# Kernel optimization log

Measured on AMD Instinct MI355X. Metric: run time of the kernel, lower is better.

The kernel has to match this reference:

```python
import jax, jax.numpy as jnp
import numpy as np

B, S, D, H, L = 32, 2048, 256, 256, 2  # batch, seq_len, input_size, hidden_size, num_layers


def setup_inputs() -> dict:
    key = jax.random.key(0)
    ks = jax.random.split(key, 11)
    s = 0.05
    return {
        "x": jax.random.normal(ks[0], (B, S, D), jnp.float32),
        "enc_h": jax.random.normal(ks[1], (B, 2 * H), jnp.float32),
        "enc_c": jax.random.normal(ks[2], (B, 2 * H), jnp.float32),
        # stacked per-layer LSTMCell params, PyTorch gate order (i, f, g, o)
        "Wih_f": jax.random.normal(ks[3], (L, 4 * H, D), jnp.float32) * s,
        "Whh_f": jax.random.normal(ks[4], (L, 4 * H, H), jnp.float32) * s,
        "bih_f": jax.random.normal(ks[5], (L, 4 * H), jnp.float32) * s,
        "bhh_f": jax.random.normal(ks[6], (L, 4 * H), jnp.float32) * s,
        "Wih_b": jax.random.normal(ks[7], (L, 4 * H, D), jnp.float32) * s,
        "Whh_b": jax.random.normal(ks[8], (L, 4 * H, H), jnp.float32) * s,
        "bih_b": jax.random.normal(ks[9], (L, 4 * H), jnp.float32) * s,
        "bhh_b": jax.random.normal(ks[10], (L, 4 * H), jnp.float32) * s,
    }


def _lstm_cell(x, h, c, Wih, Whh, b):
    gates = x @ Wih.T + h @ Whh.T + b  # [B, 4H]
    i, f, g, o = jnp.split(gates, 4, axis=-1)
    c_new = jax.nn.sigmoid(f) * c + jax.nn.sigmoid(i) * jnp.tanh(g)
    h_new = jax.nn.sigmoid(o) * jnp.tanh(c_new)
    return h_new, c_new


def reference(x, enc_h, enc_c, Wih_f, Whh_f, bih_f, bhh_f, Wih_b, Whh_b, bih_b, bhh_b):
    h = enc_h.shape[1] // 2
    nl = Wih_f.shape[0]
    # initial states: same encoder slice replicated to every layer
    hf0 = jnp.broadcast_to(enc_h[:, :h], (nl, enc_h.shape[0], h))
    hb0 = jnp.broadcast_to(enc_h[:, h:], (nl, enc_h.shape[0], h))
    cf0 = jnp.broadcast_to(enc_c[:, :h], (nl, enc_c.shape[0], h))
    cb0 = jnp.broadcast_to(enc_c[:, h:], (nl, enc_c.shape[0], h))

    def step(carry, x_t):
        hf, cf, hb, cb = carry  # each [L, B, H]
        inp_f = x_t
        inp_b = x_t[:, ::-1]  # source flips the FEATURE axis of the timestep
        hfs, cfs, hbs, cbs = [], [], [], []
        for j in range(nl):
            h_f, c_f = _lstm_cell(inp_f, hf[j], cf[j], Wih_f[j], Whh_f[j], bih_f[j] + bhh_f[j])
            h_b, c_b = _lstm_cell(inp_b, hb[j], cb[j], Wih_b[j], Whh_b[j], bih_b[j] + bhh_b[j])
            inp_f, inp_b = h_f, h_b
            hfs.append(h_f); cfs.append(c_f); hbs.append(h_b); cbs.append(c_b)
        new_carry = (jnp.stack(hfs), jnp.stack(cfs), jnp.stack(hbs), jnp.stack(cbs))
        return new_carry, jnp.concatenate([hfs[-1], hbs[-1]], axis=1)  # [B, 2H]

    carry0 = (hf0, cf0, hb0, cb0)
    xs = jnp.swapaxes(x, 0, 1)  # [S, B, D]
    (hf, cf, hb, cb), out = jax.lax.scan(step, carry0, xs)
    out = jnp.swapaxes(out, 0, 1)  # [B, S, 2H]
    h_last = jnp.concatenate([hf[-1], hb[-1]], axis=1)
    c_last = jnp.concatenate([cf[-1], cb[-1]], axis=1)
    return out, (h_last, c_last)
```

## Files before the change

kernel.cpp:

```cpp
#include <hip/hip_runtime.h>


typedef _Float16 half8 __attribute__((ext_vector_type(8)));
typedef float f32x4 __attribute__((ext_vector_type(4)));

#define B_ 32
#define S_ 2048
#define D_ 256
#define H_ 256
#define G_ 1024
#define NSLOT 8
#define OUT0 (B_*S_*2*H_)

__device__ __forceinline__ float sigmoidf_(float v){ return 1.f/(1.f+__expf(-v)); }
__device__ __forceinline__ float tanhf_(float v){ return 2.f/(1.f+__expf(-2.f*v)) - 1.f; }

union H8U { half8 h; unsigned u[4]; };

__device__ __forceinline__ half8 ld_h8_sys(const _Float16* p) {
  const unsigned* u = (const unsigned*)p;
  H8U r;
  r.u[0] = __hip_atomic_load(u+0, __ATOMIC_RELAXED, __HIP_MEMORY_SCOPE_SYSTEM);
  r.u[1] = __hip_atomic_load(u+1, __ATOMIC_RELAXED, __HIP_MEMORY_SCOPE_SYSTEM);
  r.u[2] = __hip_atomic_load(u+2, __ATOMIC_RELAXED, __HIP_MEMORY_SCOPE_SYSTEM);
  r.u[3] = __hip_atomic_load(u+3, __ATOMIC_RELAXED, __HIP_MEMORY_SCOPE_SYSTEM);
  return r.h;
}

__global__ __launch_bounds__(256) void lstm_prep(const float* __restrict__ enc_h,
                                                 int* __restrict__ flags,
                                                 _Float16* __restrict__ hbuf)
{
  int idx = blockIdx.x*blockDim.x + threadIdx.x;
  if (idx < 4*32)
    __hip_atomic_store(&flags[idx*16], 0, __ATOMIC_RELAXED, __HIP_MEMORY_SCOPE_SYSTEM);
  const int total = 4*B_*H_/2;
  for (int i = idx; i < total; i += gridDim.x*blockDim.x) {
    int di    = i*2;
    int chain = di >> 13;
    int r     = di & 8191;
    int b     = r >> 8;
    int col   = r & 255;
    int dir   = chain >> 1;
    _Float16 lo = (_Float16)enc_h[b*(2*H_) + dir*H_ + col];
    _Float16 hi = (_Float16)enc_h[b*(2*H_) + dir*H_ + col + 1];
    unsigned u = (unsigned)__builtin_bit_cast(unsigned short, lo)
               | ((unsigned)__builtin_bit_cast(unsigned short, hi) << 16);
    __hip_atomic_store((unsigned*)(hbuf + (size_t)chain*(NSLOT*B_*H_) + r), u,
                       __ATOMIC_RELAXED, __HIP_MEMORY_SCOPE_SYSTEM);
  }
}

__global__ __launch_bounds__(64,1) void lstm_main(
    const float* __restrict__ x,
    const float* __restrict__ enc_c,
    const float* __restrict__ Wih_f, const float* __restrict__ Whh_f,
    const float* __restrict__ bih_f, const float* __restrict__ bhh_f,
    const float* __restrict__ Wih_b, const float* __restrict__ Whh_b,
    const float* __restrict__ bih_b, const float* __restrict__ bhh_b,
    float* __restrict__ out,
    int* __restrict__ flags,
    _Float16* __restrict__ hbuf)
{
  const int bid   = blockIdx.x;
  const int chain = bid & 3;
  const int w     = bid >> 2;
  const int dir   = chain >> 1;
  const int layer = chain & 1;
  const int m     = w & 1;
  const int c0    = (w >> 1) << 4;
  const int lane  = threadIdx.x;
  const int quad  = lane >> 4;
  const int lq    = lane & 15;

  const float* Wih = dir ? Wih_b : Wih_f;
  const float* Whh = dir ? Whh_b : Whh_f;
  const float* bih = dir ? bih_b : bih_f;
  const float* bhh = dir ? bhh_b : bhh_f;

  half8 bf[4][16];
#pragma unroll
  for (int q = 0; q < 4; ++q) {
    const int n_g = q*256 + c0 + lq;
    const float* wihr = Wih + (size_t)layer*G_*256 + (size_t)n_g*256 + quad*8;
    const float* whhr = Whh + (size_t)layer*G_*256 + (size_t)n_g*256 + quad*8;
#pragma unroll
    for (int kk = 0; kk < 16; ++kk) {
      const float* src = (kk < 8) ? (wihr + kk*32) : (whhr + (kk-8)*32);
      f32x4 w0 = *(const f32x4*)src;
      f32x4 w1 = *(const f32x4*)(src+4);
      half8 hv;
      hv[0]=(_Float16)w0[0]; hv[1]=(_Float16)w0[1]; hv[2]=(_Float16)w0[2]; hv[3]=(_Float16)w0[3];
      hv[4]=(_Float16)w1[0]; hv[5]=(_Float16)w1[1]; hv[6]=(_Float16)w1[2]; hv[7]=(_Float16)w1[3];
      bf[q][kk] = hv;
    }
  }

  float bias[4];
#pragma unroll
  for (int q = 0; q < 4; ++q) {
    const int n_g = q*256 + c0 + lq;
    bias[q] = bih[layer*G_ + n_g] + bhh[layer*G_ + n_g];
  }

  f32x4 cst;
#pragma unroll
  for (int r = 0; r < 4; ++r) {
    const int b = m*16 + quad*4 + r;
    cst[r] = enc_c[b*(2*H_) + dir*H_ + c0 + lq];
  }

  _Float16* hbufOwn      = hbuf + (size_t)chain*(NSLOT*B_*H_);
  const _Float16* hbufL0 = hbuf + (size_t)(dir*2)*(NSLOT*B_*H_);
  int* myFlag = flags + (size_t)(chain*32 + w)*16;
  const int otherChain = (layer == 1) ? (dir*2) : (dir*2 + 1);

  const int c16 = lane & 15;
  const int grp = (lane >> 4) & 1;
  const int spinChain = grp ? otherChain : chain;
  const int* spinPtr = flags + (size_t)(spinChain*32 + (m + 2*c16))*16;
  const int tgtOff = (layer == 0) ? (grp ? -7 : 0) : (grp ? 1 : 0);

  const int arow = m*16 + lq;
  const float* xrowBase = x + (size_t)arow*S_*D_;

  bool dead = false;

  for (int t = 0; t < S_; ++t) {
    half8 ain[8], arec[8];

    if (layer == 0) {
      const float* xr = xrowBase + (size_t)t*D_;
#pragma unroll
      for (int kk = 0; kk < 8; ++kk) {
        const int k = kk*32 + quad*8;
        half8 hv;
        if (dir == 0) {
          f32x4 a0 = *(const f32x4*)(xr + k);
          f32x4 a1 = *(const f32x4*)(xr + k + 4);
          hv[0]=(_Float16)a0[0]; hv[1]=(_Float16)a0[1]; hv[2]=(_Float16)a0[2]; hv[3]=(_Float16)a0[3];
          hv[4]=(_Float16)a1[0]; hv[5]=(_Float16)a1[1]; hv[6]=(_Float16)a1[2]; hv[7]=(_Float16)a1[3];
        } else {
          const float* p = xr + (248 - k);
          f32x4 a0 = *(const f32x4*)p;
          f32x4 a1 = *(const f32x4*)(p + 4);
          hv[0]=(_Float16)a1[3]; hv[1]=(_Float16)a1[2]; hv[2]=(_Float16)a1[1]; hv[3]=(_Float16)a1[0];
          hv[4]=(_Float16)a0[3]; hv[5]=(_Float16)a0[2]; hv[6]=(_Float16)a0[1]; hv[7]=(_Float16)a0[0];
        }
        ain[kk] = hv;
      }
    }

    {
      const int tgt = t + tgtOff;
      int guard = 0;
      while (true) {
        int v = __hip_atomic_load(spinPtr, __ATOMIC_RELAXED, __HIP_MEMORY_SCOPE_SYSTEM);
        if (__all(v >= tgt)) break;
        if (++guard > (1 << 20)) { dead = true; break; }
      }
    }
    if (dead) break;
    asm volatile("" ::: "memory");

    if (layer == 0) {
      const _Float16* hs = hbufOwn + (size_t)(t & 7)*(B_*H_) + (size_t)arow*H_ + quad*8;
#pragma unroll
      for (int kk = 0; kk < 8; ++kk)
        arec[kk] = ld_h8_sys(hs + kk*32);
    } else {
      const _Float16* hi = hbufL0 + (size_t)((t+1) & 7)*(B_*H_) + (size_t)arow*H_ + quad*8;
      const _Float16* hr = hbufOwn + (size_t)(t & 7)*(B_*H_) + (size_t)arow*H_ + quad*8;
#pragma unroll
      for (int kk = 0; kk < 8; ++kk) {
        ain[kk]  = ld_h8_sys(hi + kk*32);
        arec[kk] = ld_h8_sys(hr + kk*32);
      }
    }

    f32x4 acc0 = {bias[0],bias[0],bias[0],bias[0]};
    f32x4 acc1 = {bias[1],bias[1],bias[1],bias[1]};
    f32x4 acc2 = {bias[2],bias[2],bias[2],bias[2]};
    f32x4 acc3 = {bias[3],bias[3],bias[3],bias[3]};
#pragma unroll
    for (int kk = 0; kk < 8; ++kk) {
      acc0 = __builtin_amdgcn_mfma_f32_16x16x32_f16(ain[kk], bf[0][kk], acc0, 0,0,0);
      acc1 = __builtin_amdgcn_mfma_f32_16x16x32_f16(ain[kk], bf[1][kk], acc1, 0,0,0);
      acc2 = __builtin_amdgcn_mfma_f32_16x16x32_f16(ain[kk], bf[2][kk], acc2, 0,0,0);
      acc3 = __builtin_amdgcn_mfma_f32_16x16x32_f16(ain[kk], bf[3][kk], acc3, 0,0,0);
    }
#pragma unroll
    for (int kk = 0; kk < 8; ++kk) {
      acc0 = __builtin_amdgcn_mfma_f32_16x16x32_f16(arec[kk], bf[0][kk+8], acc0, 0,0,0);
      acc1 = __builtin_amdgcn_mfma_f32_16x16x32_f16(arec[kk], bf[1][kk+8], acc1, 0,0,0);
      acc2 = __builtin_amdgcn_mfma_f32_16x16x32_f16(arec[kk], bf[2][kk+8], acc2, 0,0,0);
      acc3 = __builtin_amdgcn_mfma_f32_16x16x32_f16(arec[kk], bf[3][kk+8], acc3, 0,0,0);
    }

    float hval[4];
#pragma unroll
    for (int r = 0; r < 4; ++r) {
      float si = sigmoidf_(acc0[r]);
      float sf = sigmoidf_(acc1[r]);
      float tg = tanhf_  (acc2[r]);
      float so = sigmoidf_(acc3[r]);
      float cn = sf*cst[r] + si*tg;
      cst[r] = cn;
      hval[r] = so*tanhf_(cn);
    }

    _Float16* hw = hbufOwn + (size_t)((t+1) & 7)*(B_*H_) + c0 + lq;
#pragma unroll
    for (int r = 0; r < 4; ++r) {
      float partner = __shfl_xor(hval[r], 1);
      if (!(lq & 1)) {
        unsigned short lo = __builtin_bit_cast(unsigned short, (_Float16)hval[r]);
        unsigned short hi = __builtin_bit_cast(unsigned short, (_Float16)partner);
        unsigned u = (unsigned)lo | ((unsigned)hi << 16);
        const int b = m*16 + quad*4 + r;
        __hip_atomic_store((unsigned*)(hw + (size_t)b*H_), u,
                           __ATOMIC_RELAXED, __HIP_MEMORY_SCOPE_SYSTEM);
      }
    }
    asm volatile("s_waitcnt vmcnt(0)" ::: "memory");
    if (lane == 0)
      __hip_atomic_store(myFlag, t+1, __ATOMIC_RELAXED, __HIP_MEMORY_SCOPE_SYSTEM);

    if (layer == 1) {
      const int colg = dir*256 + c0 + lq;
#pragma unroll
      for (int r = 0; r < 4; ++r) {
        const int b = m*16 + quad*4 + r;
        out[((size_t)b*S_ + t)*(2*H_) + colg] = hval[r];
      }
      if (t == S_-1) {
#pragma unroll
        for (int r = 0; r < 4; ++r) {
          const int b = m*16 + quad*4 + r;
          out[OUT0 + (size_t)b*(2*H_) + colg] = hval[r];
          out[OUT0 + B_*2*H_ + (size_t)b*(2*H_) + colg] = cst[r];
        }
      }
    }
  }
}

extern "C" void kernel_launch(void* const* d_in, const int* in_sizes, int n_in,
                              void* d_out, int out_size, void* d_ws, size_t ws_size,
                              hipStream_t stream) {
  const float* x     = (const float*)d_in[0];
  const float* enc_h = (const float*)d_in[1];
  const float* enc_c = (const float*)d_in[2];
  const float* Wih_f = (const float*)d_in[3];
  const float* Whh_f = (const float*)d_in[4];
  const float* bih_f = (const float*)d_in[5];
  const float* bhh_f = (const float*)d_in[6];
  const float* Wih_b = (const float*)d_in[7];
  const float* Whh_b = (const float*)d_in[8];
  const float* bih_b = (const float*)d_in[9];
  const float* bhh_b = (const float*)d_in[10];

  int* flags      = (int*)d_ws;
  _Float16* hbuf  = (_Float16*)((char*)d_ws + 8192);

  lstm_prep<<<64, 256, 0, stream>>>(enc_h, flags, hbuf);
  lstm_main<<<128, 64, 0, stream>>>(x, enc_c, Wih_f, Whh_f, bih_f, bhh_f,
                                    Wih_b, Whh_b, bih_b, bhh_b,
                                    (float*)d_out, flags, hbuf);
}
```

Baseline: 13.26 ms.

## Place each synchronizing LSTM group on one XCC and use device-scope flag polling

```diff
diff --git a/kernel.cpp b/kernel.cpp
--- a/kernel.cpp
+++ b/kernel.cpp
@@ -11,6 +11,10 @@
 #define G_ 1024
 #define NSLOT 8
 #define OUT0 (B_*S_*2*H_)
+
+#define HB_SLOT   (16*H_)
+#define HB_LAYER  (NSLOT*HB_SLOT)
+#define HB_REGION (2*HB_LAYER)
 
 __device__ __forceinline__ float sigmoidf_(float v){ return 1.f/(1.f+__expf(-v)); }
 __device__ __forceinline__ float tanhf_(float v){ return 2.f/(1.f+__expf(-2.f*v)) - 1.f; }
@@ -27,56 +31,83 @@
   return r.h;
 }
 
+__device__ __forceinline__ int ld_flag_fast(const int* p) {
+  int v;
+  asm volatile("global_load_dword %0, %1, off sc0\n\ts_waitcnt vmcnt(0)"
+               : "=v"(v) : "v"(p) : "memory");
+  return v;
+}
+__device__ __forceinline__ void st_dw_fast(unsigned* p, unsigned v) {
+  asm volatile("global_store_dword %0, %1, off sc0" :: "v"(p), "v"(v) : "memory");
+}
+
+template<bool FFAST>
+__device__ __forceinline__ int flag_poll(const int* p) {
+  if constexpr (FFAST) return ld_flag_fast(p);
+  else return __hip_atomic_load(p, __ATOMIC_RELAXED, __HIP_MEMORY_SCOPE_SYSTEM);
+}
+template<bool FFAST>
+__device__ __forceinline__ void flag_raise(int* p, int v) {
+  if constexpr (FFAST) st_dw_fast((unsigned*)p, (unsigned)v);
+  else __hip_atomic_store(p, v, __ATOMIC_RELAXED, __HIP_MEMORY_SCOPE_SYSTEM);
+}
+
 __global__ __launch_bounds__(256) void lstm_prep(const float* __restrict__ enc_h,
                                                  int* __restrict__ flags,
+                                                 int* __restrict__ cnt,
+                                                 int* __restrict__ epoch,
+                                                 int* __restrict__ toks,
+                                                 int* __restrict__ verd,
                                                  _Float16* __restrict__ hbuf)
 {
   int idx = blockIdx.x*blockDim.x + threadIdx.x;
-  if (idx < 4*32)
+  if (idx == 0)
+    __hip_atomic_fetch_add(epoch, 1, __ATOMIC_RELAXED, __HIP_MEMORY_SCOPE_SYSTEM);
+  if (idx < 128) {
     __hip_atomic_store(&flags[idx*16], 0, __ATOMIC_RELAXED, __HIP_MEMORY_SCOPE_SYSTEM);
-  const int total = 4*B_*H_/2;
-  for (int i = idx; i < total; i += gridDim.x*blockDim.x) {
-    int di    = i*2;
-    int chain = di >> 13;
-    int r     = di & 8191;
-    int b     = r >> 8;
-    int col   = r & 255;
-    int dir   = chain >> 1;
+    __hip_atomic_store(&toks[idx], 0,  __ATOMIC_RELAXED, __HIP_MEMORY_SCOPE_SYSTEM);
+    __hip_atomic_store(&verd[idx], -1, __ATOMIC_RELAXED, __HIP_MEMORY_SCOPE_SYSTEM);
+  }
+  if (idx < 8)
+    __hip_atomic_store(&cnt[idx], 0, __ATOMIC_RELAXED, __HIP_MEMORY_SCOPE_SYSTEM);
+
+  for (int j = idx; j < 4*2*16*128; j += gridDim.x*blockDim.x) {
+    int c2     = j & 127;
+    int row    = (j >> 7) & 15;
+    int layer  = (j >> 11) & 1;
+    int region = j >> 12;
+    int m   = region & 1;
+    int dir = region >> 1;
+    int b   = m*16 + row;
+    int col = c2*2;
     _Float16 lo = (_Float16)enc_h[b*(2*H_) + dir*H_ + col];
     _Float16 hi = (_Float16)enc_h[b*(2*H_) + dir*H_ + col + 1];
     unsigned u = (unsigned)__builtin_bit_cast(unsigned short, lo)
                | ((unsigned)__builtin_bit_cast(unsigned short, hi) << 16);
-    __hip_atomic_store((unsigned*)(hbuf + (size_t)chain*(NSLOT*B_*H_) + r), u,
+    __hip_atomic_store((unsigned*)(hbuf + (size_t)region*HB_REGION
+                                   + (size_t)layer*HB_LAYER + row*H_ + col), u,
                        __ATOMIC_RELAXED, __HIP_MEMORY_SCOPE_SYSTEM);
   }
 }
 
-__global__ __launch_bounds__(64,1) void lstm_main(
+template<bool FFAST>
+__device__ __forceinline__ void run_lstm(
     const float* __restrict__ x,
     const float* __restrict__ enc_c,
-    const float* __restrict__ Wih_f, const float* __restrict__ Whh_f,
-    const float* __restrict__ bih_f, const float* __restrict__ bhh_f,
-    const float* __restrict__ Wih_b, const float* __restrict__ Whh_b,
-    const float* __restrict__ bih_b, const float* __restrict__ bhh_b,
+    const float* __restrict__ Wih, const float* __restrict__ Whh,
+    const float* __restrict__ bih, const float* __restrict__ bhh,
     float* __restrict__ out,
     int* __restrict__ flags,
-    _Float16* __restrict__ hbuf)
+    _Float16* __restrict__ hbuf,
+    int region, int member)
 {
-  const int bid   = blockIdx.x;
-  const int chain = bid & 3;
-  const int w     = bid >> 2;
-  const int dir   = chain >> 1;
-  const int layer = chain & 1;
-  const int m     = w & 1;
-  const int c0    = (w >> 1) << 4;
+  const int dir   = region >> 1;
+  const int m     = region & 1;
+  const int layer = member & 1;
+  const int c0    = (member >> 1) << 4;
   const int lane  = threadIdx.x;
   const int quad  = lane >> 4;
   const int lq    = lane & 15;
-
-  const float* Wih = dir ? Wih_b : Wih_f;
-  const float* Whh = dir ? Whh_b : Whh_f;
-  const float* bih = dir ? bih_b : bih_f;
-  const float* bhh = dir ? bhh_b : bhh_f;
 
   half8 bf[4][16];
 #pragma unroll
@@ -110,19 +141,21 @@
     cst[r] = enc_c[b*(2*H_) + dir*H_ + c0 + lq];
   }
 
-  _Float16* hbufOwn      = hbuf + (size_t)chain*(NSLOT*B_*H_);
-  const _Float16* hbufL0 = hbuf + (size_t)(dir*2)*(NSLOT*B_*H_);
-  int* myFlag = flags + (size_t)(chain*32 + w)*16;
-  const int otherChain = (layer == 1) ? (dir*2) : (dir*2 + 1);
+  _Float16* hbR          = hbuf + (size_t)region*HB_REGION;
+  _Float16* hbufOwn      = hbR + (size_t)layer*HB_LAYER;
+  const _Float16* hbufL0 = hbR;
+  int* flagsR = flags + region*(32*16);
+  int* myFlag = flagsR + member*16;
 
   const int c16 = lane & 15;
   const int grp = (lane >> 4) & 1;
-  const int spinChain = grp ? otherChain : chain;
-  const int* spinPtr = flags + (size_t)(spinChain*32 + (m + 2*c16))*16;
+  const int spinLayer = grp ? (layer ^ 1) : layer;
+  const int* spinPtr = flagsR + (c16*2 + spinLayer)*16;
   const int tgtOff = (layer == 0) ? (grp ? -7 : 0) : (grp ? 1 : 0);
 
   const int arow = m*16 + lq;
   const float* xrowBase = x + (size_t)arow*S_*D_;
+  const bool writer = (layer == 1);
 
   bool dead = false;
 
@@ -155,7 +188,7 @@
       const int tgt = t + tgtOff;
       int guard = 0;
       while (true) {
-        int v = __hip_atomic_load(spinPtr, __ATOMIC_RELAXED, __HIP_MEMORY_SCOPE_SYSTEM);
+        int v = flag_poll<FFAST>(spinPtr);
         if (__all(v >= tgt)) break;
         if (++guard > (1 << 20)) { dead = true; break; }
       }
@@ -164,13 +197,13 @@
     asm volatile("" ::: "memory");
 
     if (layer == 0) {
-      const _Float16* hs = hbufOwn + (size_t)(t & 7)*(B_*H_) + (size_t)arow*H_ + quad*8;
+      const _Float16* hs = hbufOwn + (size_t)(t & 7)*HB_SLOT + (size_t)lq*H_ + quad*8;
 #pragma unroll
       for (int kk = 0; kk < 8; ++kk)
         arec[kk] = ld_h8_sys(hs + kk*32);
     } else {
-      const _Float16* hi = hbufL0 + (size_t)((t+1) & 7)*(B_*H_) + (size_t)arow*H_ + quad*8;
-      const _Float16* hr = hbufOwn + (size_t)(t & 7)*(B_*H_) + (size_t)arow*H_ + quad*8;
+      const _Float16* hi = hbufL0 + (size_t)((t+1) & 7)*HB_SLOT + (size_t)lq*H_ + quad*8;
+      const _Float16* hr = hbufOwn + (size_t)(t & 7)*HB_SLOT + (size_t)lq*H_ + quad*8;
 #pragma unroll
       for (int kk = 0; kk < 8; ++kk) {
         ain[kk]  = ld_h8_sys(hi + kk*32);
@@ -209,7 +242,7 @@
       hval[r] = so*tanhf_(cn);
     }
 
-    _Float16* hw = hbufOwn + (size_t)((t+1) & 7)*(B_*H_) + c0 + lq;
+    _Float16* hw = hbufOwn + (size_t)((t+1) & 7)*HB_SLOT + c0 + lq;
 #pragma unroll
     for (int r = 0; r < 4; ++r) {
       float partner = __shfl_xor(hval[r], 1);
@@ -217,16 +250,16 @@
         unsigned short lo = __builtin_bit_cast(unsigned short, (_Float16)hval[r]);
         unsigned short hi = __builtin_bit_cast(unsigned short, (_Float16)partner);
         unsigned u = (unsigned)lo | ((unsigned)hi << 16);
-        const int b = m*16 + quad*4 + r;
-        __hip_atomic_store((unsigned*)(hw + (size_t)b*H_), u,
+        const int bl = quad*4 + r;
+        __hip_atomic_store((unsigned*)(hw + (size_t)bl*H_), u,
                            __ATOMIC_RELAXED, __HIP_MEMORY_SCOPE_SYSTEM);
       }
     }
     asm volatile("s_waitcnt vmcnt(0)" ::: "memory");
     if (lane == 0)
-      __hip_atomic_store(myFlag, t+1, __ATOMIC_RELAXED, __HIP_MEMORY_SCOPE_SYSTEM);
-
-    if (layer == 1) {
+      flag_raise<FFAST>(myFlag, t+1);
+
+    if (writer) {
       const int colg = dir*256 + c0 + lq;
 #pragma unroll
       for (int r = 0; r < 4; ++r) {
@@ -243,6 +276,81 @@
       }
     }
   }
+}
+
+__global__ __launch_bounds__(64,1) void lstm_main(
+    const float* __restrict__ x,
+    const float* __restrict__ enc_c,
+    const float* __restrict__ Wih_f, const float* __restrict__ Whh_f,
+    const float* __restrict__ bih_f, const float* __restrict__ bhh_f,
+    const float* __restrict__ Wih_b, const float* __restrict__ Whh_b,
+    const float* __restrict__ bih_b, const float* __restrict__ bhh_b,
+    float* __restrict__ out,
+    int* __restrict__ flags,
+    int* __restrict__ cnt,
+    int* __restrict__ epoch,
+    int* __restrict__ toks,
+    int* __restrict__ verd,
+    _Float16* __restrict__ hbuf)
+{
+  unsigned xcc;
+  asm volatile("s_getreg_b32 %0, hwreg(HW_REG_XCC_ID)" : "=s"(xcc));
+  xcc &= 7;
+  if (xcc >= 4) return;
+  const int region = (int)xcc;
+  const int lane = threadIdx.x;
+
+  int tk = 0;
+  if (lane == 0)
+    tk = __hip_atomic_fetch_add(cnt + region, 1, __ATOMIC_RELAXED,
+                                __HIP_MEMORY_SCOPE_SYSTEM);
+  tk = __shfl(tk, 0);
+  if (tk >= 32) return;
+  const int member = tk;
+
+  const unsigned E = (unsigned)__hip_atomic_load(epoch, __ATOMIC_RELAXED,
+                                                 __HIP_MEMORY_SCOPE_SYSTEM);
+
+  int* tokR = toks + region*32;
+  bool ok = true;
+#pragma unroll 1
+  for (int phase = 1; phase <= 2; ++phase) {
+    const unsigned tgt = E*2u + (unsigned)phase;
+    if (lane == 0) st_dw_fast((unsigned*)&tokR[member], tgt);
+    int guard = 0;
+    while (true) {
+      int v = ld_flag_fast(&tokR[lane & 31]);
+      if (__all((int)((unsigned)v - tgt) >= 0)) break;
+      if (++guard > (1 << 17)) { ok = false; break; }
+    }
+    if (!ok) break;
+  }
+
+  if (lane == 0)
+    __hip_atomic_store(&verd[region*32 + member], ok ? 1 : 0,
+                       __ATOMIC_RELAXED, __HIP_MEMORY_SCOPE_SYSTEM);
+  int vd = -1; bool have = true;
+  {
+    int guard = 0;
+    while (true) {
+      vd = __hip_atomic_load(&verd[region*32 + (lane & 31)],
+                             __ATOMIC_RELAXED, __HIP_MEMORY_SCOPE_SYSTEM);
+      if (__all(vd >= 0)) break;
+      if (++guard > (1 << 18)) { have = false; break; }
+    }
+  }
+  const bool fast = have && __all(vd == 1);
+
+  const int dir = region >> 1;
+  const float* Wih = dir ? Wih_b : Wih_f;
+  const float* Whh = dir ? Whh_b : Whh_f;
+  const float* bih = dir ? bih_b : bih_f;
+  const float* bhh = dir ? bhh_b : bhh_f;
+
+  if (fast)
+    run_lstm<true >(x, enc_c, Wih, Whh, bih, bhh, out, flags, hbuf, region, member);
+  else
+    run_lstm<false>(x, enc_c, Wih, Whh, bih, bhh, out, flags, hbuf, region, member);
 }
 
 extern "C" void kernel_launch(void* const* d_in, const int* in_sizes, int n_in,
@@ -260,11 +368,15 @@
   const float* bih_b = (const float*)d_in[9];
   const float* bhh_b = (const float*)d_in[10];
 
-  int* flags      = (int*)d_ws;
-  _Float16* hbuf  = (_Float16*)((char*)d_ws + 8192);
-
-  lstm_prep<<<64, 256, 0, stream>>>(enc_h, flags, hbuf);
-  lstm_main<<<128, 64, 0, stream>>>(x, enc_c, Wih_f, Whh_f, bih_f, bhh_f,
+  int* flags     = (int*)d_ws;
+  int* cnt       = (int*)((char*)d_ws + 8192);
+  int* epoch     = (int*)((char*)d_ws + 8448);
+  int* toks      = (int*)((char*)d_ws + 8704);
+  int* verd      = (int*)((char*)d_ws + 9728);
+  _Float16* hbuf = (_Float16*)((char*)d_ws + 32768);
+
+  lstm_prep<<<64, 256, 0, stream>>>(enc_h, flags, cnt, epoch, toks, verd, hbuf);
+  lstm_main<<<512, 64, 0, stream>>>(x, enc_c, Wih_f, Whh_f, bih_f, bhh_f,
                                     Wih_b, Whh_b, bih_b, bhh_b,
-                                    (float*)d_out, flags, hbuf);
-}
+                                    (float*)d_out, flags, cnt, epoch, toks, verd, hbuf);
+}
```

New measurement: 26.46 ms. 99.5% more time.

## Group four waves per block to cut cross-block flag polling

Applied to the files above, without the earlier changes.

```diff
diff --git a/kernel.cpp b/kernel.cpp
--- a/kernel.cpp
+++ b/kernel.cpp
@@ -11,6 +11,9 @@
 #define G_ 1024
 #define NSLOT 8
 #define OUT0 (B_*S_*2*H_)
+
+#define SLOT_F16 (16*64)
+#define BLK_F16  (NSLOT*SLOT_F16)
 
 __device__ __forceinline__ float sigmoidf_(float v){ return 1.f/(1.f+__expf(-v)); }
 __device__ __forceinline__ float tanhf_(float v){ return 2.f/(1.f+__expf(-2.f*v)) - 1.f; }
@@ -32,26 +35,27 @@
                                                  _Float16* __restrict__ hbuf)
 {
   int idx = blockIdx.x*blockDim.x + threadIdx.x;
-  if (idx < 4*32)
+  if (idx < 32)
     __hip_atomic_store(&flags[idx*16], 0, __ATOMIC_RELAXED, __HIP_MEMORY_SCOPE_SYSTEM);
-  const int total = 4*B_*H_/2;
-  for (int i = idx; i < total; i += gridDim.x*blockDim.x) {
-    int di    = i*2;
-    int chain = di >> 13;
-    int r     = di & 8191;
-    int b     = r >> 8;
-    int col   = r & 255;
-    int dir   = chain >> 1;
-    _Float16 lo = (_Float16)enc_h[b*(2*H_) + dir*H_ + col];
-    _Float16 hi = (_Float16)enc_h[b*(2*H_) + dir*H_ + col + 1];
+  for (int j = idx; j < 32*16*32; j += gridDim.x*blockDim.x) {
+    int c2  = j & 31;
+    int row = (j >> 5) & 15;
+    int blk = j >> 9;
+    int Q   = blk & 3;
+    int m   = (blk >> 2) & 1;
+    int dir = blk >> 4;
+    int b    = m*16 + row;
+    int gcol = Q*64 + c2*2;
+    _Float16 lo = (_Float16)enc_h[b*(2*H_) + dir*H_ + gcol];
+    _Float16 hi = (_Float16)enc_h[b*(2*H_) + dir*H_ + gcol + 1];
     unsigned u = (unsigned)__builtin_bit_cast(unsigned short, lo)
                | ((unsigned)__builtin_bit_cast(unsigned short, hi) << 16);
-    __hip_atomic_store((unsigned*)(hbuf + (size_t)chain*(NSLOT*B_*H_) + r), u,
+    __hip_atomic_store((unsigned*)(hbuf + (size_t)blk*BLK_F16 + row*64 + c2*2), u,
                        __ATOMIC_RELAXED, __HIP_MEMORY_SCOPE_SYSTEM);
   }
 }
 
-__global__ __launch_bounds__(64,1) void lstm_main(
+__global__ __launch_bounds__(256,1) void lstm_main(
     const float* __restrict__ x,
     const float* __restrict__ enc_c,
     const float* __restrict__ Wih_f, const float* __restrict__ Whh_f,
@@ -62,14 +66,14 @@
     int* __restrict__ flags,
     _Float16* __restrict__ hbuf)
 {
-  const int bid   = blockIdx.x;
-  const int chain = bid & 3;
-  const int w     = bid >> 2;
-  const int dir   = chain >> 1;
-  const int layer = chain & 1;
-  const int m     = w & 1;
-  const int c0    = (w >> 1) << 4;
-  const int lane  = threadIdx.x;
+  const int blk   = blockIdx.x;
+  const int Q     = blk & 3;
+  const int m     = (blk >> 2) & 1;
+  const int layer = (blk >> 3) & 1;
+  const int dir   = blk >> 4;
+  const int tid   = threadIdx.x;
+  const int wv    = tid >> 6;
+  const int lane  = tid & 63;
   const int quad  = lane >> 4;
   const int lq    = lane & 15;
 
@@ -78,10 +82,12 @@
   const float* bih = dir ? bih_b : bih_f;
   const float* bhh = dir ? bhh_b : bhh_f;
 
+  const int gbase = Q*64 + wv*16;
+
   half8 bf[4][16];
 #pragma unroll
   for (int q = 0; q < 4; ++q) {
-    const int n_g = q*256 + c0 + lq;
+    const int n_g = q*256 + gbase + lq;
     const float* wihr = Wih + (size_t)layer*G_*256 + (size_t)n_g*256 + quad*8;
     const float* whhr = Whh + (size_t)layer*G_*256 + (size_t)n_g*256 + quad*8;
 #pragma unroll
@@ -99,7 +105,7 @@
   float bias[4];
 #pragma unroll
   for (int q = 0; q < 4; ++q) {
-    const int n_g = q*256 + c0 + lq;
+    const int n_g = q*256 + gbase + lq;
     bias[q] = bih[layer*G_ + n_g] + bhh[layer*G_ + n_g];
   }
 
@@ -107,24 +113,26 @@
 #pragma unroll
   for (int r = 0; r < 4; ++r) {
     const int b = m*16 + quad*4 + r;
-    cst[r] = enc_c[b*(2*H_) + dir*H_ + c0 + lq];
-  }
-
-  _Float16* hbufOwn      = hbuf + (size_t)chain*(NSLOT*B_*H_);
-  const _Float16* hbufL0 = hbuf + (size_t)(dir*2)*(NSLOT*B_*H_);
-  int* myFlag = flags + (size_t)(chain*32 + w)*16;
-  const int otherChain = (layer == 1) ? (dir*2) : (dir*2 + 1);
-
-  const int c16 = lane & 15;
-  const int grp = (lane >> 4) & 1;
-  const int spinChain = grp ? otherChain : chain;
-  const int* spinPtr = flags + (size_t)(spinChain*32 + (m + 2*c16))*16;
-  const int tgtOff = (layer == 0) ? (grp ? -7 : 0) : (grp ? 1 : 0);
+    cst[r] = enc_c[b*(2*H_) + dir*H_ + gbase + lq];
+  }
+
+  const int sameBase  = (dir<<4) | (layer<<3) | (m<<2);
+  const int otherBase = sameBase ^ 8;
+  _Float16* ownBlk = hbuf + (size_t)blk*BLK_F16;
+  int* myFlag = flags + blk*16;
+
+  int fblk, tgtOff;
+  if (lane < 3)      { fblk = sameBase  + ((Q + 1 + lane) & 3); tgtOff = 0; }
+  else if (lane < 7) { fblk = otherBase + (lane - 3); tgtOff = layer ? 1 : -7; }
+  else               { fblk = sameBase  + ((Q + 1) & 3); tgtOff = 0; }
+  const int* spinPtr = flags + fblk*16;
+
+  __shared__ int ldsDead;
+  if (tid == 0) ldsDead = 0;
+  __syncthreads();
 
   const int arow = m*16 + lq;
   const float* xrowBase = x + (size_t)arow*S_*D_;
-
-  bool dead = false;
 
   for (int t = 0; t < S_; ++t) {
     half8 ain[8], arec[8];
@@ -157,24 +165,27 @@
       while (true) {
         int v = __hip_atomic_load(spinPtr, __ATOMIC_RELAXED, __HIP_MEMORY_SCOPE_SYSTEM);
         if (__all(v >= tgt)) break;
-        if (++guard > (1 << 20)) { dead = true; break; }
-      }
-    }
-    if (dead) break;
+        if (++guard > (1 << 18)) { ldsDead = 1; break; }
+      }
+    }
     asm volatile("" ::: "memory");
 
-    if (layer == 0) {
-      const _Float16* hs = hbufOwn + (size_t)(t & 7)*(B_*H_) + (size_t)arow*H_ + quad*8;
-#pragma unroll
-      for (int kk = 0; kk < 8; ++kk)
-        arec[kk] = ld_h8_sys(hs + kk*32);
-    } else {
-      const _Float16* hi = hbufL0 + (size_t)((t+1) & 7)*(B_*H_) + (size_t)arow*H_ + quad*8;
-      const _Float16* hr = hbufOwn + (size_t)(t & 7)*(B_*H_) + (size_t)arow*H_ + quad*8;
+#pragma unroll
+    for (int kk = 0; kk < 8; ++kk) {
+      const int qq = kk >> 1;
+      const _Float16* p = hbuf + (size_t)(sameBase + qq)*BLK_F16
+                        + (size_t)(t & 7)*SLOT_F16
+                        + (size_t)lq*64 + (kk & 1)*32 + quad*8;
+      arec[kk] = ld_h8_sys(p);
+    }
+    if (layer == 1) {
 #pragma unroll
       for (int kk = 0; kk < 8; ++kk) {
-        ain[kk]  = ld_h8_sys(hi + kk*32);
-        arec[kk] = ld_h8_sys(hr + kk*32);
+        const int qq = kk >> 1;
+        const _Float16* p = hbuf + (size_t)(otherBase + qq)*BLK_F16
+                          + (size_t)((t+1) & 7)*SLOT_F16
+                          + (size_t)lq*64 + (kk & 1)*32 + quad*8;
+        ain[kk] = ld_h8_sys(p);
       }
     }
 
@@ -209,7 +220,7 @@
       hval[r] = so*tanhf_(cn);
     }
 
-    _Float16* hw = hbufOwn + (size_t)((t+1) & 7)*(B_*H_) + c0 + lq;
+    _Float16* hw = ownBlk + (size_t)((t+1) & 7)*SLOT_F16 + wv*16 + lq;
 #pragma unroll
     for (int r = 0; r < 4; ++r) {
       float partner = __shfl_xor(hval[r], 1);
@@ -217,17 +228,18 @@
         unsigned short lo = __builtin_bit_cast(unsigned short, (_Float16)hval[r]);
         unsigned short hi = __builtin_bit_cast(unsigned short, (_Float16)partner);
         unsigned u = (unsigned)lo | ((unsigned)hi << 16);
-        const int b = m*16 + quad*4 + r;
-        __hip_atomic_store((unsigned*)(hw + (size_t)b*H_), u,
+        const int bl = quad*4 + r;
+        __hip_atomic_store((unsigned*)(hw + (size_t)bl*64), u,
                            __ATOMIC_RELAXED, __HIP_MEMORY_SCOPE_SYSTEM);
       }
     }
     asm volatile("s_waitcnt vmcnt(0)" ::: "memory");
-    if (lane == 0)
+    __syncthreads();
+    if (tid == 0)
       __hip_atomic_store(myFlag, t+1, __ATOMIC_RELAXED, __HIP_MEMORY_SCOPE_SYSTEM);
 
     if (layer == 1) {
-      const int colg = dir*256 + c0 + lq;
+      const int colg = dir*256 + gbase + lq;
 #pragma unroll
       for (int r = 0; r < 4; ++r) {
         const int b = m*16 + quad*4 + r;
@@ -242,6 +254,8 @@
         }
       }
     }
+
+    if (ldsDead) break;
   }
 }
 
@@ -260,11 +274,11 @@
   const float* bih_b = (const float*)d_in[9];
   const float* bhh_b = (const float*)d_in[10];
 
-  int* flags      = (int*)d_ws;
-  _Float16* hbuf  = (_Float16*)((char*)d_ws + 8192);
+  int* flags     = (int*)d_ws;
+  _Float16* hbuf = (_Float16*)((char*)d_ws + 32768);
 
   lstm_prep<<<64, 256, 0, stream>>>(enc_h, flags, hbuf);
-  lstm_main<<<128, 64, 0, stream>>>(x, enc_c, Wih_f, Whh_f, bih_f, bhh_f,
+  lstm_main<<<32, 256, 0, stream>>>(x, enc_c, Wih_f, Whh_f, bih_f, bhh_f,
                                     Wih_b, Whh_b, bih_b, bhh_b,
                                     (float*)d_out, flags, hbuf);
 }
```

Result: slower. 18.86 ms (+42.2%).

## Replace per-wave flags with epoch-tagged 64-bit data packets for step sync

Applied to the files above, without the earlier changes.

```diff
diff --git a/kernel.cpp b/kernel.cpp
--- a/kernel.cpp
+++ b/kernel.cpp
@@ -3,51 +3,57 @@
 
 typedef _Float16 half8 __attribute__((ext_vector_type(8)));
 typedef float f32x4 __attribute__((ext_vector_type(4)));
+typedef unsigned u32x4v __attribute__((ext_vector_type(4)));
+typedef unsigned long long ull;
 
 #define B_ 32
 #define S_ 2048
 #define D_ 256
 #define H_ 256
 #define G_ 1024
-#define NSLOT 8
 #define OUT0 (B_*S_*2*H_)
+
+#define NSLOT 4
+#define PKTROW 128
+
+__device__ __forceinline__ size_t hoff(int chain, int slot, int row, int pkt){
+  return ((size_t)((chain*NSLOT + slot)*B_ + row))*PKTROW + pkt;
+}
 
 __device__ __forceinline__ float sigmoidf_(float v){ return 1.f/(1.f+__expf(-v)); }
 __device__ __forceinline__ float tanhf_(float v){ return 2.f/(1.f+__expf(-2.f*v)) - 1.f; }
 
-union H8U { half8 h; unsigned u[4]; };
-
-__device__ __forceinline__ half8 ld_h8_sys(const _Float16* p) {
-  const unsigned* u = (const unsigned*)p;
-  H8U r;
-  r.u[0] = __hip_atomic_load(u+0, __ATOMIC_RELAXED, __HIP_MEMORY_SCOPE_SYSTEM);
-  r.u[1] = __hip_atomic_load(u+1, __ATOMIC_RELAXED, __HIP_MEMORY_SCOPE_SYSTEM);
-  r.u[2] = __hip_atomic_load(u+2, __ATOMIC_RELAXED, __HIP_MEMORY_SCOPE_SYSTEM);
-  r.u[3] = __hip_atomic_load(u+3, __ATOMIC_RELAXED, __HIP_MEMORY_SCOPE_SYSTEM);
-  return r.h;
+__device__ __forceinline__ ull ld_pkt(const ull* p){
+  return __hip_atomic_load(p, __ATOMIC_RELAXED, __HIP_MEMORY_SCOPE_SYSTEM);
+}
+__device__ __forceinline__ void st_pkt(ull* p, ull v){
+  __hip_atomic_store(p, v, __ATOMIC_RELAXED, __HIP_MEMORY_SCOPE_SYSTEM);
+}
+
+__global__ __launch_bounds__(64) void epoch_bump(unsigned* __restrict__ epoch)
+{
+  if (threadIdx.x == 0)
+    __hip_atomic_fetch_add(epoch, 1u, __ATOMIC_RELAXED, __HIP_MEMORY_SCOPE_SYSTEM);
 }
 
 __global__ __launch_bounds__(256) void lstm_prep(const float* __restrict__ enc_h,
-                                                 int* __restrict__ flags,
-                                                 _Float16* __restrict__ hbuf)
+                                                 const unsigned* __restrict__ epoch,
+                                                 ull* __restrict__ hb)
 {
+  const unsigned tag0 = __hip_atomic_load(epoch, __ATOMIC_RELAXED,
+                                          __HIP_MEMORY_SCOPE_SYSTEM) * 4096u;
   int idx = blockIdx.x*blockDim.x + threadIdx.x;
-  if (idx < 4*32)
-    __hip_atomic_store(&flags[idx*16], 0, __ATOMIC_RELAXED, __HIP_MEMORY_SCOPE_SYSTEM);
-  const int total = 4*B_*H_/2;
-  for (int i = idx; i < total; i += gridDim.x*blockDim.x) {
-    int di    = i*2;
-    int chain = di >> 13;
-    int r     = di & 8191;
-    int b     = r >> 8;
-    int col   = r & 255;
-    int dir   = chain >> 1;
-    _Float16 lo = (_Float16)enc_h[b*(2*H_) + dir*H_ + col];
-    _Float16 hi = (_Float16)enc_h[b*(2*H_) + dir*H_ + col + 1];
-    unsigned u = (unsigned)__builtin_bit_cast(unsigned short, lo)
-               | ((unsigned)__builtin_bit_cast(unsigned short, hi) << 16);
-    __hip_atomic_store((unsigned*)(hbuf + (size_t)chain*(NSLOT*B_*H_) + r), u,
-                       __ATOMIC_RELAXED, __HIP_MEMORY_SCOPE_SYSTEM);
+  for (int j = idx; j < 4*B_*PKTROW; j += gridDim.x*blockDim.x) {
+    int pkt   = j & 127;
+    int row   = (j >> 7) & 31;
+    int chain = j >> 12;
+    int dirv  = chain >> 1;
+    int col   = pkt*2;
+    _Float16 lo = (_Float16)enc_h[row*(2*H_) + dirv*H_ + col];
+    _Float16 hi = (_Float16)enc_h[row*(2*H_) + dirv*H_ + col + 1];
+    unsigned pair = (unsigned)__builtin_bit_cast(unsigned short, lo)
+                  | ((unsigned)__builtin_bit_cast(unsigned short, hi) << 16);
+    st_pkt(hb + hoff(chain, 0, row, pkt), ((ull)tag0 << 32) | pair);
   }
 }
 
@@ -59,8 +65,8 @@
     const float* __restrict__ Wih_b, const float* __restrict__ Whh_b,
     const float* __restrict__ bih_b, const float* __restrict__ bhh_b,
     float* __restrict__ out,
-    int* __restrict__ flags,
-    _Float16* __restrict__ hbuf)
+    const unsigned* __restrict__ epoch,
+    ull* __restrict__ hb)
 {
   const int bid   = blockIdx.x;
   const int chain = bid & 3;
@@ -110,16 +116,13 @@
     cst[r] = enc_c[b*(2*H_) + dir*H_ + c0 + lq];
   }
 
-  _Float16* hbufOwn      = hbuf + (size_t)chain*(NSLOT*B_*H_);
-  const _Float16* hbufL0 = hbuf + (size_t)(dir*2)*(NSLOT*B_*H_);
-  int* myFlag = flags + (size_t)(chain*32 + w)*16;
-  const int otherChain = (layer == 1) ? (dir*2) : (dir*2 + 1);
-
-  const int c16 = lane & 15;
-  const int grp = (lane >> 4) & 1;
-  const int spinChain = grp ? otherChain : chain;
-  const int* spinPtr = flags + (size_t)(spinChain*32 + (m + 2*c16))*16;
-  const int tgtOff = (layer == 0) ? (grp ? -7 : 0) : (grp ? 1 : 0);
+  const unsigned EB = __hip_atomic_load(epoch, __ATOMIC_RELAXED,
+                                        __HIP_MEMORY_SCOPE_SYSTEM) * 4096u;
+
+  const int  pm        = lane & 15;
+  const int  probeRow  = m*16 + 15;
+  const int  probePkt  = pm*8 + 7;
+  const bool probeAlt  = ((lane >> 4) & 1) != 0;
 
   const int arow = m*16 + lq;
   const float* xrowBase = x + (size_t)arow*S_*D_;
@@ -128,6 +131,7 @@
 
   for (int t = 0; t < S_; ++t) {
     half8 ain[8], arec[8];
+    const unsigned tagT = EB + (unsigned)t;
 
     if (layer == 0) {
       const float* xr = xrowBase + (size_t)t*D_;
@@ -152,30 +156,55 @@
     }
 
     {
-      const int tgt = t + tgtOff;
+      const ull* pp;
+      unsigned want;
+      bool isGE = false;
+      if (layer == 0) {
+        if (!probeAlt) { pp = hb + hoff(chain,   t&3,     probeRow, probePkt); want = tagT; }
+        else           { pp = hb + hoff(chain+1, (t+1)&3, probeRow, probePkt); want = tagT - 3; isGE = true; }
+      } else {
+        if (!probeAlt) { pp = hb + hoff(chain,   t&3,     probeRow, probePkt); want = tagT; }
+        else           { pp = hb + hoff(chain-1, (t+1)&3, probeRow, probePkt); want = tagT + 1; }
+      }
       int guard = 0;
       while (true) {
-        int v = __hip_atomic_load(spinPtr, __ATOMIC_RELAXED, __HIP_MEMORY_SCOPE_SYSTEM);
-        if (__all(v >= tgt)) break;
-        if (++guard > (1 << 20)) { dead = true; break; }
-      }
-    }
-    if (dead) break;
-    asm volatile("" ::: "memory");
-
-    if (layer == 0) {
-      const _Float16* hs = hbufOwn + (size_t)(t & 7)*(B_*H_) + (size_t)arow*H_ + quad*8;
-#pragma unroll
-      for (int kk = 0; kk < 8; ++kk)
-        arec[kk] = ld_h8_sys(hs + kk*32);
-    } else {
-      const _Float16* hi = hbufL0 + (size_t)((t+1) & 7)*(B_*H_) + (size_t)arow*H_ + quad*8;
-      const _Float16* hr = hbufOwn + (size_t)(t & 7)*(B_*H_) + (size_t)arow*H_ + quad*8;
-#pragma unroll
-      for (int kk = 0; kk < 8; ++kk) {
-        ain[kk]  = ld_h8_sys(hi + kk*32);
-        arec[kk] = ld_h8_sys(hr + kk*32);
-      }
+        unsigned tg = (unsigned)(ld_pkt(pp) >> 32);
+        bool ok = isGE ? ((t < 3) || ((int)(tg - want) >= 0)) : (tg == want);
+        if (__all(ok)) break;
+        if (++guard > (1 << 19)) { dead = true; break; }
+      }
+      if (dead) break;
+    }
+
+    {
+      int guard = 0;
+      while (true) {
+        bool ok = true;
+#pragma unroll
+        for (int kk = 0; kk < 8; ++kk) {
+          const ull* p4 = hb + hoff(chain, t&3, arow, kk*16 + quad*4);
+          ull p0 = ld_pkt(p4+0), p1 = ld_pkt(p4+1), p2 = ld_pkt(p4+2), p3 = ld_pkt(p4+3);
+          ok &= ((unsigned)(p0>>32) == tagT) & ((unsigned)(p1>>32) == tagT)
+              & ((unsigned)(p2>>32) == tagT) & ((unsigned)(p3>>32) == tagT);
+          u32x4v d = { (unsigned)p0, (unsigned)p1, (unsigned)p2, (unsigned)p3 };
+          arec[kk] = __builtin_bit_cast(half8, d);
+        }
+        if (layer == 1) {
+          const unsigned tagU = tagT + 1;
+#pragma unroll
+          for (int kk = 0; kk < 8; ++kk) {
+            const ull* p4 = hb + hoff(chain-1, (t+1)&3, arow, kk*16 + quad*4);
+            ull p0 = ld_pkt(p4+0), p1 = ld_pkt(p4+1), p2 = ld_pkt(p4+2), p3 = ld_pkt(p4+3);
+            ok &= ((unsigned)(p0>>32) == tagU) & ((unsigned)(p1>>32) == tagU)
+                & ((unsigned)(p2>>32) == tagU) & ((unsigned)(p3>>32) == tagU);
+            u32x4v d = { (unsigned)p0, (unsigned)p1, (unsigned)p2, (unsigned)p3 };
+            ain[kk] = __builtin_bit_cast(half8, d);
+          }
+        }
+        if (__all(ok)) break;
+        if (++guard > (1 << 16)) { dead = true; break; }
+      }
+      if (dead) break;
     }
 
     f32x4 acc0 = {bias[0],bias[0],bias[0],bias[0]};
@@ -209,22 +238,21 @@
       hval[r] = so*tanhf_(cn);
     }
 
-    _Float16* hw = hbufOwn + (size_t)((t+1) & 7)*(B_*H_) + c0 + lq;
-#pragma unroll
-    for (int r = 0; r < 4; ++r) {
-      float partner = __shfl_xor(hval[r], 1);
-      if (!(lq & 1)) {
-        unsigned short lo = __builtin_bit_cast(unsigned short, (_Float16)hval[r]);
-        unsigned short hi = __builtin_bit_cast(unsigned short, (_Float16)partner);
-        unsigned u = (unsigned)lo | ((unsigned)hi << 16);
-        const int b = m*16 + quad*4 + r;
-        __hip_atomic_store((unsigned*)(hw + (size_t)b*H_), u,
-                           __ATOMIC_RELAXED, __HIP_MEMORY_SCOPE_SYSTEM);
-      }
-    }
-    asm volatile("s_waitcnt vmcnt(0)" ::: "memory");
-    if (lane == 0)
-      __hip_atomic_store(myFlag, t+1, __ATOMIC_RELAXED, __HIP_MEMORY_SCOPE_SYSTEM);
+    {
+      const unsigned tagN = tagT + 1;
+#pragma unroll
+      for (int r = 0; r < 4; ++r) {
+        float partner = __shfl_xor(hval[r], 1);
+        if (!(lq & 1)) {
+          unsigned short lo = __builtin_bit_cast(unsigned short, (_Float16)hval[r]);
+          unsigned short hi = __builtin_bit_cast(unsigned short, (_Float16)partner);
+          unsigned pair = (unsigned)lo | ((unsigned)hi << 16);
+          const int row = m*16 + quad*4 + r;
+          const int pkt = (c0 + lq) >> 1;
+          st_pkt(hb + hoff(chain, (t+1)&3, row, pkt), ((ull)tagN << 32) | pair);
+        }
+      }
+    }
 
     if (layer == 1) {
       const int colg = dir*256 + c0 + lq;
@@ -260,11 +288,12 @@
   const float* bih_b = (const float*)d_in[9];
   const float* bhh_b = (const float*)d_in[10];
 
-  int* flags      = (int*)d_ws;
-  _Float16* hbuf  = (_Float16*)((char*)d_ws + 8192);
-
-  lstm_prep<<<64, 256, 0, stream>>>(enc_h, flags, hbuf);
+  unsigned* epoch = (unsigned*)((char*)d_ws + 16384);
+  ull* hb         = (ull*)((char*)d_ws + 32768);
+
+  epoch_bump<<<1, 64, 0, stream>>>(epoch);
+  lstm_prep<<<64, 256, 0, stream>>>(enc_h, epoch, hb);
   lstm_main<<<128, 64, 0, stream>>>(x, enc_c, Wih_f, Whh_f, bih_f, bhh_f,
                                     Wih_b, Whh_b, bih_b, bhh_b,
-                                    (float*)d_out, flags, hbuf);
-}
+                                    (float*)d_out, epoch, hb);
+}
```

New measurement: 14.10 ms. 1.06x slower.
